# Kernel tuning notes

Hardware: AMD Instinct MI355X
Metric: run time of the kernel (lower is better)

## Reference

```python
import jax, jax.numpy as jnp
import numpy as np

D_MODEL, N_HEAD, N_KV_HEAD, D_HEAD = 1024, 16, 4, 64


def rotate_half(x):
    x1, x2 = x[..., : x.shape[-1] // 2], x[..., x.shape[-1] // 2:]
    return jnp.concatenate((-x2, x1), axis=-1)


def rope_cos_sin(seq_len, dim, dtype=jnp.float32):
    inv_freq = 1.0 / (10000.0 ** (jnp.arange(0, dim, 2, dtype=jnp.float32) / dim))
    t = jnp.arange(seq_len, dtype=jnp.float32)
    freqs = jnp.einsum('i,j->ij', t, inv_freq)          # [S, dim/2]
    emb = jnp.concatenate((freqs, freqs), axis=-1)       # [S, dim]
    return jnp.cos(emb).astype(dtype), jnp.sin(emb).astype(dtype)


def setup_inputs() -> dict:
    key = jax.random.key(0)
    ks = jax.random.split(key, 5)
    B, S = 2, 2048
    scale = 0.02
    return {
        'x': jax.random.normal(ks[0], (B, S, D_MODEL), dtype=jnp.float32),
        'Wq': jax.random.normal(ks[1], (D_MODEL, N_HEAD * D_HEAD), dtype=jnp.float32) * scale,
        'Wk': jax.random.normal(ks[2], (D_MODEL, N_KV_HEAD * D_HEAD), dtype=jnp.float32) * scale,
        'Wv': jax.random.normal(ks[3], (D_MODEL, N_KV_HEAD * D_HEAD), dtype=jnp.float32) * scale,
        'Wo': jax.random.normal(ks[4], (N_HEAD * D_HEAD, D_MODEL), dtype=jnp.float32) * scale,
    }


def reference(x, Wq, Wk, Wv, Wo):
    B, S, _ = x.shape
    scale = 1.0 / np.sqrt(D_HEAD)
    # projections -> [B, H, S, Dh]
    q = (x @ Wq).reshape(B, S, N_HEAD, D_HEAD).transpose(0, 2, 1, 3)
    k = (x @ Wk).reshape(B, S, N_KV_HEAD, D_HEAD).transpose(0, 2, 1, 3)
    v = (x @ Wv).reshape(B, S, N_KV_HEAD, D_HEAD).transpose(0, 2, 1, 3)
    cos, sin = rope_cos_sin(S, D_HEAD, x.dtype)          # [S, Dh]
    q = q * cos + rotate_half(q) * sin
    k = k * cos + rotate_half(k) * sin
    rep = N_HEAD // N_KV_HEAD
    k = jnp.repeat(k, rep, axis=1)                       # [B, H, S, Dh]
    v = jnp.repeat(v, rep, axis=1)
    scores = jnp.einsum('bhqd,bhkd->bhqk', q, k) * scale # [B, H, S, S]
    causal = jnp.triu(jnp.ones((S, S), dtype=bool), k=1)
    scores = jnp.where(causal, -jnp.inf, scores)
    probs = jax.nn.softmax(scores, axis=-1)
    ctx = jnp.einsum('bhqk,bhkd->bhqd', probs, v)        # [B, H, S, Dh]
    ctx = ctx.transpose(0, 2, 1, 3).reshape(B, S, N_HEAD * D_HEAD)
    return ctx @ Wo
```

## Files before the change

### kernel.cpp

```cpp
#include <hip/hip_runtime.h>
#include <hip/hip_bf16.h>
#include <cstdint>
#include <math.h>

#define S_LEN 2048
#define DM 1024
#define NQKV 1536
#define MROWS 4096
#define BKT 64

typedef __attribute__((ext_vector_type(8))) short short8;
typedef __attribute__((ext_vector_type(4))) float f32x4;
typedef __attribute__((ext_vector_type(16))) float f32x16;

#define QFOLD 0.18033688011112042f

__device__ __forceinline__ short f2bf(float x) {
  union { float f; uint32_t u; } v; v.f = x;
  uint32_t r = (v.u + 0x7fffu + ((v.u >> 16) & 1u)) >> 16;
  return (short)(uint16_t)r;
}

__device__ __forceinline__ uint32_t pk2(float a, float b) {
  __hip_bfloat162 h = __float22bfloat162_rn(make_float2(a, b));
  union { __hip_bfloat162 h2; uint32_t u; } cv; cv.h2 = h;
  return cv.u;
}

__global__ __launch_bounds__(256) void prep(const float* __restrict__ x,
    const float* __restrict__ Wq, const float* __restrict__ Wk,
    const float* __restrict__ Wv, const float* __restrict__ Wo,
    short* __restrict__ Xb, short* __restrict__ WcatT, short* __restrict__ WoT,
    float2* __restrict__ tab) {
  __shared__ short T[64 * 72];
  const int bb = blockIdx.x;
  const int tid = threadIdx.x;
  if (bb < 4096) {
    const int i = bb * 256 + tid;
    float4 v = ((const float4*)x)[i];
    short4 o;
    o.x = f2bf(v.x); o.y = f2bf(v.y); o.z = f2bf(v.z); o.w = f2bf(v.w);
    ((short4*)Xb)[i] = o;
    return;
  }
  if (bb >= 4736) {
    const int gid = (bb - 4736) * 256 + tid;
    #pragma unroll
    for (int e = 0; e < 4; ++e) {
      const int ii = gid + e * 16384;
      const int s = ii >> 5, j = ii & 31;
      const float inv = exp2f(-(float)j * 0.41524101186092029f);
      const float ang = (float)s * inv;
      tab[ii] = make_float2(cosf(ang), sinf(ang));
    }
    return;
  }
  const float* src; short* dst; int R, C, t2 = bb - 4096;
  if (t2 < 256)      { src = Wq; dst = WcatT;                        R = 1024; C = 1024; }
  else if (t2 < 320) { t2 -= 256; src = Wk; dst = WcatT + (size_t)1024*1024; R = 1024; C = 256; }
  else if (t2 < 384) { t2 -= 320; src = Wv; dst = WcatT + (size_t)1280*1024; R = 1024; C = 256; }
  else               { t2 -= 384; src = Wo; dst = WoT;               R = 1024; C = 1024; }
  const int r0 = (t2 & 15) * 64, c0 = (t2 >> 4) * 64;
  #pragma unroll
  for (int i = 0; i < 4; ++i) {
    int chunk = tid + i * 256;
    int r = chunk >> 4, cc = (chunk & 15) * 4;
    float4 v = *(const float4*)&src[(size_t)(r0 + r) * C + c0 + cc];
    T[(cc + 0) * 72 + r] = f2bf(v.x);
    T[(cc + 1) * 72 + r] = f2bf(v.y);
    T[(cc + 2) * 72 + r] = f2bf(v.z);
    T[(cc + 3) * 72 + r] = f2bf(v.w);
  }
  __syncthreads();
  #pragma unroll
  for (int i = 0; i < 2; ++i) {
    int chunk = tid + i * 256;
    int rr = chunk >> 3, kk = (chunk & 7) * 8;
    *(uint4*)&dst[(size_t)(c0 + rr) * R + r0 + kk] = *(uint4*)&T[rr * 72 + kk];
  }
}

template<int BMT, int BNT>
__global__ __launch_bounds__(256) void gemm_bf16_t(const short* __restrict__ A,
    const short* __restrict__ BT, float* __restrict__ C, int M, int N, int K) {
  constexpr int MI = BMT / 32, NI = BNT / 32;
  __shared__ short As[BMT * BKT];
  __shared__ short Bs[BNT * BKT];
  const int tid = threadIdx.x;
  const int wave = tid >> 6, lane = tid & 63;
  const int quad = lane >> 4, l15 = lane & 15;
  const int wm = (wave >> 1) * (BMT / 2), wn = (wave & 1) * (BNT / 2);
  const int m0 = blockIdx.y * BMT, n0 = blockIdx.x * BNT;
  const int rA = wave * (BMT / 4) + (lane >> 3);
  const int rB = wave * (BNT / 4) + (lane >> 3);
  const int scol = (lane & 7) * 8;

  f32x4 acc[MI][NI] = {};

  for (int k0 = 0; k0 < K; k0 += BKT) {
    __syncthreads();
    #pragma unroll
    for (int j = 0; j < MI; ++j)
      __builtin_amdgcn_global_load_lds(
          (const __attribute__((address_space(1))) void*)&A[(size_t)(m0 + rA + j * 8) * K + k0 + scol],
          (__attribute__((address_space(3))) void*)&As[(wave * MI + j) * 512],
          16, 0, 0);
    #pragma unroll
    for (int j = 0; j < NI; ++j)
      __builtin_amdgcn_global_load_lds(
          (const __attribute__((address_space(1))) void*)&BT[(size_t)(n0 + rB + j * 8) * K + k0 + scol],
          (__attribute__((address_space(3))) void*)&Bs[(wave * NI + j) * 512],
          16, 0, 0);
    __syncthreads();
    #pragma unroll
    for (int ks = 0; ks < 2; ++ks) {
      short8 af[MI], bfr[NI];
      #pragma unroll
      for (int mi = 0; mi < MI; ++mi)
        af[mi] = *(const short8*)&As[(wm + mi*16 + l15)*BKT + ks*32 + quad*8];
      #pragma unroll
      for (int ni = 0; ni < NI; ++ni)
        bfr[ni] = *(const short8*)&Bs[(wn + ni*16 + l15)*BKT + ks*32 + quad*8];
      #pragma unroll
      for (int mi = 0; mi < MI; ++mi)
        #pragma unroll
        for (int ni = 0; ni < NI; ++ni)
          acc[mi][ni] = __builtin_amdgcn_mfma_f32_16x16x32_bf16(af[mi], bfr[ni], acc[mi][ni], 0, 0, 0);
    }
  }
  #pragma unroll
  for (int mi = 0; mi < MI; ++mi)
    #pragma unroll
    for (int ni = 0; ni < NI; ++ni)
      #pragma unroll
      for (int r = 0; r < 4; ++r)
        C[(size_t)(m0 + wm + mi*16 + quad*4 + r)*N + (n0 + wn + ni*16 + l15)] = acc[mi][ni][r];
}

__global__ __launch_bounds__(256, 3) void gemm_qkv(const short* __restrict__ A,
    const short* __restrict__ BT, const float2* __restrict__ tab,
    short* __restrict__ Qb, short* __restrict__ Kb, short* __restrict__ Vt) {
  constexpr int MI = 2, NI = 4;
  __shared__ short SM[12288];
  short* As = SM;
  short* Bs = SM + 4096;
  const int tid = threadIdx.x;
  const int wave = tid >> 6, lane = tid & 63;
  const int quad = lane >> 4, l15 = lane & 15;
  const int wm = (wave >> 1) * 32, wn = (wave & 1) * 64;
  const int m0 = blockIdx.y * 64, n0 = blockIdx.x * 128;
  const int rA = wave * 16 + (lane >> 3);
  const int rB = wave * 32 + (lane >> 3);
  const int scol = (lane & 7) * 8;

  f32x4 acc[MI][NI] = {};

  for (int k0 = 0; k0 < DM; k0 += BKT) {
    __syncthreads();
    #pragma unroll
    for (int j = 0; j < MI; ++j)
      __builtin_amdgcn_global_load_lds(
          (const __attribute__((address_space(1))) void*)&A[(size_t)(m0 + rA + j * 8) * DM + k0 + scol],
          (__attribute__((address_space(3))) void*)&As[(wave * MI + j) * 512],
          16, 0, 0);
    #pragma unroll
    for (int j = 0; j < NI; ++j)
      __builtin_amdgcn_global_load_lds(
          (const __attribute__((address_space(1))) void*)&BT[(size_t)(n0 + rB + j * 8) * DM + k0 + scol],
          (__attribute__((address_space(3))) void*)&Bs[(wave * NI + j) * 512],
          16, 0, 0);
    __syncthreads();
    #pragma unroll
    for (int ks = 0; ks < 2; ++ks) {
      short8 af[MI], bfr[NI];
      #pragma unroll
      for (int mi = 0; mi < MI; ++mi)
        af[mi] = *(const short8*)&As[(wm + mi*16 + l15)*BKT + ks*32 + quad*8];
      #pragma unroll
      for (int ni = 0; ni < NI; ++ni)
        bfr[ni] = *(const short8*)&Bs[(wn + ni*16 + l15)*BKT + ks*32 + quad*8];
      #pragma unroll
      for (int mi = 0; mi < MI; ++mi)
        #pragma unroll
        for (int ni = 0; ni < NI; ++ni)
          acc[mi][ni] = __builtin_amdgcn_mfma_f32_16x16x32_bf16(af[mi], bfr[ni], acc[mi][ni], 0, 0, 0);
    }
  }

  const int c0 = n0 + wn;
  if (n0 < 1024) {
    #pragma unroll
    for (int mi = 0; mi < MI; ++mi)
      #pragma unroll
      for (int r = 0; r < 4; ++r) {
        const int row = m0 + wm + mi*16 + quad*4 + r;
        const int s = row & (S_LEN - 1);
        #pragma unroll
        for (int ni = 0; ni < 2; ++ni) {
          const int j = ni*16 + l15;
          const float2 cn = tab[s*32 + j];
          const float x1 = acc[mi][ni][r], x2 = acc[mi][ni+2][r];
          Qb[(size_t)row*1024 + c0 + j]      = f2bf((x1*cn.x - x2*cn.y) * QFOLD);
          Qb[(size_t)row*1024 + c0 + j + 32] = f2bf((x2*cn.x + x1*cn.y) * QFOLD);
        }
      }
  } else if (n0 < 1280) {
    const int hh = (c0 - 1024) >> 6;
    #pragma unroll
    for (int mi = 0; mi < MI; ++mi)
      #pragma unroll
      for (int r = 0; r < 4; ++r) {
        const int row = m0 + wm + mi*16 + quad*4 + r;
        const int s = row & (S_LEN - 1);
        const int sw = (s & 7) << 3;
        #pragma unroll
        for (int ni = 0; ni < 2; ++ni) {
          const int j = ni*16 + l15;
          const float2 cn = tab[s*32 + j];
          const float x1 = acc[mi][ni][r], x2 = acc[mi][ni+2][r];
          Kb[(size_t)row*256 + hh*64 + (j ^ sw)]        = f2bf(x1*cn.x - x2*cn.y);
          Kb[(size_t)row*256 + hh*64 + ((j + 32) ^ sw)] = f2bf(x2*cn.x + x1*cn.y);
        }
      }
  } else {
    __syncthreads();
    #pragma unroll
    for (int mi = 0; mi < MI; ++mi)
      #pragma unroll
      for (int ni = 0; ni < NI; ++ni) {
        short4 p;
        p.x = f2bf(acc[mi][ni][0]); p.y = f2bf(acc[mi][ni][1]);
        p.z = f2bf(acc[mi][ni][2]); p.w = f2bf(acc[mi][ni][3]);
        *(short4*)&SM[(wn + ni*16 + l15)*80 + wm + mi*16 + quad*4] = p;
      }
    __syncthreads();
    const int b_ = m0 >> 11, sbase = m0 & (S_LEN - 1);
    #pragma unroll
    for (int i = 0; i < 4; ++i) {
      const int chunk = tid + i * 256;
      const int vl = chunk >> 3;
      const int kk = (chunk & 7) * 8;
      const int vcol = (n0 - 1280) + vl;
      const int kvh = vcol >> 6, dd = vcol & 63;
      uint4 v = *(uint4*)&SM[vl*80 + kk];
      *(uint4*)&Vt[((size_t)((b_*4 + kvh)*64 + dd))*S_LEN + sbase + (kk ^ ((dd & 7) << 3))] = v;
    }
  }
}

__global__ __launch_bounds__(256, 3) void fattn12(const short* __restrict__ Qb,
    const short* __restrict__ Kb, const short* __restrict__ Vt, short* __restrict__ Ctx) {
  __shared__ short SMEM[24576];
  const int idx = blockIdx.x;
  const int h   = idx & 15;
  const int b   = (idx >> 4) & 1;
  const int jt  = 31 - (idx >> 5);
  const int kvh = h >> 2;
  const int tid = threadIdx.x, wav = tid >> 6, lane = tid & 63;
  const int l31 = lane & 31, hi = lane >> 5;
  const int qs = wav & 1, g = wav >> 1;
  const int sx = (l31 & 7) << 3;
  const size_t qbase  = (size_t)b * S_LEN * 1024;
  const size_t kbase  = (size_t)b * S_LEN * 256;
  const size_t vtbase = (size_t)(b * 4 + kvh) * 64 * S_LEN;

  const short* kptr = Kb + kbase + (size_t)(wav * 16 + (lane >> 3)) * 256 + kvh * 64 + (lane & 7) * 8;
  const short* vptr = Vt + vtbase + (size_t)(wav * 16 + (lane >> 3)) * 2048 + (lane & 7) * 8;

#define STAGE(u) do { \
    const int bi_ = (u) % 3; \
    const short* kp_ = kptr + (size_t)(u) * 16384; \
    const short* vp_ = vptr + (u) * 64; \
    short* kd_ = &SMEM[bi_ * 8192 + wav * 1024]; \
    short* vd_ = &SMEM[bi_ * 8192 + 4096 + wav * 1024]; \
    _Pragma("unroll") \
    for (int i_ = 0; i_ < 2; ++i_) { \
      __builtin_amdgcn_global_load_lds((const __attribute__((address_space(1))) void*)(kp_ + i_ * 2048), \
          (__attribute__((address_space(3))) void*)(kd_ + i_ * 512), 16, 0, 0); \
      __builtin_amdgcn_global_load_lds((const __attribute__((address_space(1))) void*)(vp_ + i_ * 16384), \
          (__attribute__((address_space(3))) void*)(vd_ + i_ * 512), 16, 0, 0); \
    } \
  } while (0)

  const int q0 = jt * 64;
  const int ntiles = jt + 1;
  const int qg = q0 + qs * 32 + l31;

  short8 qf[4];
  {
    const short* qp = &Qb[qbase + (size_t)qg * 1024 + h * 64 + hi * 8];
    #pragma unroll
    for (int ks = 0; ks < 4; ++ks) qf[ks] = *(const short8*)(qp + ks * 16);
  }

  f32x16 O0 = {}, O1 = {};
  f32x16 P0 = {}, P1 = {};
  float la0 = 0.f, la1 = 0.f, la2 = 0.f, la3 = 0.f;

  STAGE(0);
  if (ntiles > 1) STAGE(1);

  for (int t = 0; t < ntiles; ++t) {
    const int k0 = t * 64;
    const int rem = ntiles - 1 - t;
    if (rem >= 1) { asm volatile("s_waitcnt vmcnt(4)" ::: "memory"); }
    else          { asm volatile("s_waitcnt vmcnt(0)" ::: "memory"); }
    __builtin_amdgcn_sched_barrier(0);
    __builtin_amdgcn_s_barrier();
    if (t + 2 < ntiles) STAGE(t + 2);

    const short* ks_ = &SMEM[(t % 3) * 8192];
    const short* vs_ = &SMEM[(t % 3) * 8192 + 4096];

    f32x16 sc;
    __builtin_amdgcn_s_setprio(1);
    {
      const int r = g * 32 + l31;
      short8 kf0 = *(const short8*)&ks_[r * 64 + ((0 * 16 + hi * 8) ^ sx)];
      short8 kf1 = *(const short8*)&ks_[r * 64 + ((1 * 16 + hi * 8) ^ sx)];
      short8 kf2 = *(const short8*)&ks_[r * 64 + ((2 * 16 + hi * 8) ^ sx)];
      short8 kf3 = *(const short8*)&ks_[r * 64 + ((3 * 16 + hi * 8) ^ sx)];
      f32x16 a0 = {}, a1 = {};
      a0 = __builtin_amdgcn_mfma_f32_32x32x16_bf16(kf0, qf[0], a0, 0, 0, 0);
      a1 = __builtin_amdgcn_mfma_f32_32x32x16_bf16(kf2, qf[2], a1, 0, 0, 0);
      a0 = __builtin_amdgcn_mfma_f32_32x32x16_bf16(kf1, qf[1], a0, 0, 0, 0);
      a1 = __builtin_amdgcn_mfma_f32_32x32x16_bf16(kf3, qf[3], a1, 0, 0, 0);
      #pragma unroll
      for (int r2 = 0; r2 < 16; ++r2) sc[r2] = a0[r2] + a1[r2];
    }
    __builtin_amdgcn_s_setprio(0);

    if (t == ntiles - 1) {
      #pragma unroll
      for (int r = 0; r < 16; ++r) {
        const int kvg = k0 + g * 32 + (r & 3) + 8 * (r >> 2) + 4 * hi;
        if (kvg > qg) sc[r] = -1e30f;
      }
    }

    short8 af[2];
    {
      #pragma unroll
      for (int r = 0; r < 16; ++r) sc[r] = exp2f(sc[r]);
      la0 += (sc[0] + sc[1]) + (sc[2] + sc[3]);
      la1 += (sc[4] + sc[5]) + (sc[6] + sc[7]);
      la2 += (sc[8] + sc[9]) + (sc[10] + sc[11]);
      la3 += (sc[12] + sc[13]) + (sc[14] + sc[15]);
      #pragma unroll
      for (int st = 0; st < 2; ++st) {
        uint32_t x0 = pk2(sc[st * 8 + 0], sc[st * 8 + 1]);
        uint32_t x1 = pk2(sc[st * 8 + 2], sc[st * 8 + 3]);
        uint32_t x2 = pk2(sc[st * 8 + 4], sc[st * 8 + 5]);
        uint32_t x3 = pk2(sc[st * 8 + 6], sc[st * 8 + 7]);
        asm("v_permlane32_swap_b32 %0, %1" : "+v"(x0), "+v"(x2));
        asm("v_permlane32_swap_b32 %0, %1" : "+v"(x1), "+v"(x3));
        union { short8 s8; uint32_t u[4]; } cv;
        cv.u[0] = x0; cv.u[1] = x1; cv.u[2] = x2; cv.u[3] = x3;
        af[st] = cv.s8;
      }
    }

    __builtin_amdgcn_s_setprio(1);
    {
      const int co0 = g * 32 + hi * 8;
      const int co1 = g * 32 + 16 + hi * 8;
      short8 bv00 = *(const short8*)&vs_[l31 * 64 + (co0 ^ sx)];
      short8 bv01 = *(const short8*)&vs_[(32 + l31) * 64 + (co0 ^ sx)];
      short8 bv10 = *(const short8*)&vs_[l31 * 64 + (co1 ^ sx)];
      short8 bv11 = *(const short8*)&vs_[(32 + l31) * 64 + (co1 ^ sx)];
      O0 = __builtin_amdgcn_mfma_f32_32x32x16_bf16(af[0], bv00, O0, 0, 0, 0);
      O1 = __builtin_amdgcn_mfma_f32_32x32x16_bf16(af[0], bv01, O1, 0, 0, 0);
      P0 = __builtin_amdgcn_mfma_f32_32x32x16_bf16(af[1], bv10, P0, 0, 0, 0);
      P1 = __builtin_amdgcn_mfma_f32_32x32x16_bf16(af[1], bv11, P1, 0, 0, 0);
    }
    __builtin_amdgcn_s_setprio(0);
  }

  #pragma unroll
  for (int r = 0; r < 16; ++r) { O0[r] += P0[r]; O1[r] += P1[r]; }

  float ll = (la0 + la1) + (la2 + la3);
  ll += __shfl_xor(ll, 32, 64);
  __syncthreads();

  float* Os = (float*)SMEM;
  float* Ls = (float*)SMEM + 2 * 64 * 33;
  if (g == 1) {
    float* op = &Os[(qs * 64 + lane) * 33];
    #pragma unroll
    for (int r = 0; r < 16; ++r) { op[r] = O0[r]; op[16 + r] = O1[r]; }
    Ls[qs * 64 + lane] = ll;
  }
  __syncthreads();
  if (g == 0) {
    const float* op = &Os[(qs * 64 + lane) * 33];
    ll += Ls[qs * 64 + lane];
    #pragma unroll
    for (int r = 0; r < 16; ++r) { O0[r] += op[r]; O1[r] += op[16 + r]; }
    const float inv = 1.0f / ll;
    #pragma unroll
    for (int r = 0; r < 16; ++r) {
      const int crow = (r & 3) + 8 * (r >> 2) + 4 * hi;
      const float invr = __shfl(inv, crow, 64);
      const size_t o = qbase + (size_t)(q0 + qs * 32 + crow) * 1024 + h * 64;
      Ctx[o + l31]      = f2bf(O0[r] * invr);
      Ctx[o + 32 + l31] = f2bf(O1[r] * invr);
    }
  }
#undef STAGE
}

extern "C" void kernel_launch(void* const* d_in, const int* in_sizes, int n_in,
                              void* d_out, int out_size, void* d_ws, size_t ws_size,
                              hipStream_t stream) {
  const float* x  = (const float*)d_in[0];
  const float* Wq = (const float*)d_in[1];
  const float* Wk = (const float*)d_in[2];
  const float* Wv = (const float*)d_in[3];
  const float* Wo = (const float*)d_in[4];
  float* out = (float*)d_out;

  char* w = (char*)d_ws;
  short*  Xb    = (short*)w;   w += (size_t)MROWS * DM * 2;
  short*  WcatT = (short*)w;   w += (size_t)NQKV * DM * 2;
  short*  WoT   = (short*)w;   w += (size_t)DM * DM * 2;
  short*  Qbuf  = (short*)w;   w += (size_t)MROWS * DM * 2;
  short*  Kbuf  = (short*)w;   w += (size_t)MROWS * 256 * 2;
  short*  Vt    = (short*)w;   w += (size_t)8 * 64 * S_LEN * 2;
  short*  Ctx   = (short*)w;   w += (size_t)MROWS * DM * 2;
  float2* tab   = (float2*)w;  w += (size_t)S_LEN * 32 * 8;

  prep<<<dim3(4800), dim3(256), 0, stream>>>(x, Wq, Wk, Wv, Wo, Xb, WcatT, WoT, tab);

  gemm_qkv<<<dim3(NQKV / 128, MROWS / 64), dim3(256), 0, stream>>>(Xb, WcatT, tab, Qbuf, Kbuf, Vt);
  fattn12<<<dim3(1024), dim3(256), 0, stream>>>(Qbuf, Kbuf, Vt, Ctx);
  gemm_bf16_t<64,128><<<dim3(DM / 128, MROWS / 64), dim3(256), 0, stream>>>(Ctx, WoT, out, MROWS, DM, DM);
}
```

Measured before the change: 164.2 us.

## Share KV tiles across the four GQA query heads in one attention block

```diff
diff --git a/kernel.cpp b/kernel.cpp
--- a/kernel.cpp
+++ b/kernel.cpp
@@ -248,43 +248,43 @@
   }
 }
 
-__global__ __launch_bounds__(256, 3) void fattn12(const short* __restrict__ Qb,
+__global__ __launch_bounds__(256, 3) void fattn13(const short* __restrict__ Qb,
     const short* __restrict__ Kb, const short* __restrict__ Vt, short* __restrict__ Ctx) {
   __shared__ short SMEM[24576];
   const int idx = blockIdx.x;
-  const int h   = idx & 15;
-  const int b   = (idx >> 4) & 1;
-  const int jt  = 31 - (idx >> 5);
-  const int kvh = h >> 2;
+  const int kk_ = (idx & 255) >> 3;
+  const int jt  = (idx >> 8) ? kk_ : 63 - kk_;
+  const int b   = (idx >> 2) & 1;
+  const int kvh = idx & 3;
   const int tid = threadIdx.x, wav = tid >> 6, lane = tid & 63;
   const int l31 = lane & 31, hi = lane >> 5;
-  const int qs = wav & 1, g = wav >> 1;
+  const int h = kvh * 4 + wav;
   const int sx = (l31 & 7) << 3;
   const size_t qbase  = (size_t)b * S_LEN * 1024;
   const size_t kbase  = (size_t)b * S_LEN * 256;
   const size_t vtbase = (size_t)(b * 4 + kvh) * 64 * S_LEN;
 
-  const short* kptr = Kb + kbase + (size_t)(wav * 16 + (lane >> 3)) * 256 + kvh * 64 + (lane & 7) * 8;
-  const short* vptr = Vt + vtbase + (size_t)(wav * 16 + (lane >> 3)) * 2048 + (lane & 7) * 8;
+  const short* kptr = Kb + kbase + (size_t)(tid >> 3) * 256 + kvh * 64 + (tid & 7) * 8;
+  const short* vptr = Vt + vtbase + (size_t)(tid >> 3) * 2048 + (tid & 7) * 8;
 
 #define STAGE(u) do { \
     const int bi_ = (u) % 3; \
     const short* kp_ = kptr + (size_t)(u) * 16384; \
     const short* vp_ = vptr + (u) * 64; \
-    short* kd_ = &SMEM[bi_ * 8192 + wav * 1024]; \
-    short* vd_ = &SMEM[bi_ * 8192 + 4096 + wav * 1024]; \
+    short* kd_ = &SMEM[bi_ * 8192 + tid * 8]; \
+    short* vd_ = &SMEM[bi_ * 8192 + 4096 + tid * 8]; \
     _Pragma("unroll") \
     for (int i_ = 0; i_ < 2; ++i_) { \
-      __builtin_amdgcn_global_load_lds((const __attribute__((address_space(1))) void*)(kp_ + i_ * 2048), \
-          (__attribute__((address_space(3))) void*)(kd_ + i_ * 512), 16, 0, 0); \
-      __builtin_amdgcn_global_load_lds((const __attribute__((address_space(1))) void*)(vp_ + i_ * 16384), \
-          (__attribute__((address_space(3))) void*)(vd_ + i_ * 512), 16, 0, 0); \
+      __builtin_amdgcn_global_load_lds((const __attribute__((address_space(1))) void*)(kp_ + i_ * 8192), \
+          (__attribute__((address_space(3))) void*)(kd_ + i_ * 2048), 16, 0, 0); \
+      __builtin_amdgcn_global_load_lds((const __attribute__((address_space(1))) void*)(vp_ + i_ * 65536), \
+          (__attribute__((address_space(3))) void*)(vd_ + i_ * 2048), 16, 0, 0); \
     } \
   } while (0)
 
-  const int q0 = jt * 64;
-  const int ntiles = jt + 1;
-  const int qg = q0 + qs * 32 + l31;
+  const int q0 = jt * 32;
+  const int ntiles = (jt >> 1) + 1;
+  const int qg = q0 + l31;
 
   short8 qf[4];
   {
@@ -294,7 +294,6 @@
   }
 
   f32x16 O0 = {}, O1 = {};
-  f32x16 P0 = {}, P1 = {};
   float la0 = 0.f, la1 = 0.f, la2 = 0.f, la3 = 0.f;
 
   STAGE(0);
@@ -312,100 +311,76 @@
     const short* ks_ = &SMEM[(t % 3) * 8192];
     const short* vs_ = &SMEM[(t % 3) * 8192 + 4096];
 
-    f32x16 sc;
+    f32x16 sc[2];
     __builtin_amdgcn_s_setprio(1);
-    {
-      const int r = g * 32 + l31;
-      short8 kf0 = *(const short8*)&ks_[r * 64 + ((0 * 16 + hi * 8) ^ sx)];
-      short8 kf1 = *(const short8*)&ks_[r * 64 + ((1 * 16 + hi * 8) ^ sx)];
-      short8 kf2 = *(const short8*)&ks_[r * 64 + ((2 * 16 + hi * 8) ^ sx)];
-      short8 kf3 = *(const short8*)&ks_[r * 64 + ((3 * 16 + hi * 8) ^ sx)];
-      f32x16 a0 = {}, a1 = {};
-      a0 = __builtin_amdgcn_mfma_f32_32x32x16_bf16(kf0, qf[0], a0, 0, 0, 0);
-      a1 = __builtin_amdgcn_mfma_f32_32x32x16_bf16(kf2, qf[2], a1, 0, 0, 0);
-      a0 = __builtin_amdgcn_mfma_f32_32x32x16_bf16(kf1, qf[1], a0, 0, 0, 0);
-      a1 = __builtin_amdgcn_mfma_f32_32x32x16_bf16(kf3, qf[3], a1, 0, 0, 0);
-      #pragma unroll
-      for (int r2 = 0; r2 < 16; ++r2) sc[r2] = a0[r2] + a1[r2];
+    #pragma unroll
+    for (int kt = 0; kt < 2; ++kt) {
+      const int r = kt * 32 + l31;
+      f32x16 a = {};
+      #pragma unroll
+      for (int ks2 = 0; ks2 < 4; ++ks2) {
+        short8 kf = *(const short8*)&ks_[r * 64 + ((ks2 * 16 + hi * 8) ^ sx)];
+        a = __builtin_amdgcn_mfma_f32_32x32x16_bf16(kf, qf[ks2], a, 0, 0, 0);
+      }
+      sc[kt] = a;
     }
     __builtin_amdgcn_s_setprio(0);
 
     if (t == ntiles - 1) {
       #pragma unroll
-      for (int r = 0; r < 16; ++r) {
-        const int kvg = k0 + g * 32 + (r & 3) + 8 * (r >> 2) + 4 * hi;
-        if (kvg > qg) sc[r] = -1e30f;
-      }
-    }
-
-    short8 af[2];
-    {
-      #pragma unroll
-      for (int r = 0; r < 16; ++r) sc[r] = exp2f(sc[r]);
-      la0 += (sc[0] + sc[1]) + (sc[2] + sc[3]);
-      la1 += (sc[4] + sc[5]) + (sc[6] + sc[7]);
-      la2 += (sc[8] + sc[9]) + (sc[10] + sc[11]);
-      la3 += (sc[12] + sc[13]) + (sc[14] + sc[15]);
+      for (int kt = 0; kt < 2; ++kt)
+        #pragma unroll
+        for (int r = 0; r < 16; ++r) {
+          const int kvg = k0 + kt * 32 + (r & 3) + 8 * (r >> 2) + 4 * hi;
+          if (kvg > qg) sc[kt][r] = -1e30f;
+        }
+    }
+
+    short8 af[4];
+    #pragma unroll
+    for (int kt = 0; kt < 2; ++kt) {
+      #pragma unroll
+      for (int r = 0; r < 16; ++r) sc[kt][r] = exp2f(sc[kt][r]);
+      la0 += (sc[kt][0] + sc[kt][1]) + (sc[kt][2] + sc[kt][3]);
+      la1 += (sc[kt][4] + sc[kt][5]) + (sc[kt][6] + sc[kt][7]);
+      la2 += (sc[kt][8] + sc[kt][9]) + (sc[kt][10] + sc[kt][11]);
+      la3 += (sc[kt][12] + sc[kt][13]) + (sc[kt][14] + sc[kt][15]);
       #pragma unroll
       for (int st = 0; st < 2; ++st) {
-        uint32_t x0 = pk2(sc[st * 8 + 0], sc[st * 8 + 1]);
-        uint32_t x1 = pk2(sc[st * 8 + 2], sc[st * 8 + 3]);
-        uint32_t x2 = pk2(sc[st * 8 + 4], sc[st * 8 + 5]);
-        uint32_t x3 = pk2(sc[st * 8 + 6], sc[st * 8 + 7]);
+        uint32_t x0 = pk2(sc[kt][st * 8 + 0], sc[kt][st * 8 + 1]);
+        uint32_t x1 = pk2(sc[kt][st * 8 + 2], sc[kt][st * 8 + 3]);
+        uint32_t x2 = pk2(sc[kt][st * 8 + 4], sc[kt][st * 8 + 5]);
+        uint32_t x3 = pk2(sc[kt][st * 8 + 6], sc[kt][st * 8 + 7]);
         asm("v_permlane32_swap_b32 %0, %1" : "+v"(x0), "+v"(x2));
         asm("v_permlane32_swap_b32 %0, %1" : "+v"(x1), "+v"(x3));
         union { short8 s8; uint32_t u[4]; } cv;
         cv.u[0] = x0; cv.u[1] = x1; cv.u[2] = x2; cv.u[3] = x3;
-        af[st] = cv.s8;
+        af[kt * 2 + st] = cv.s8;
       }
     }
 
     __builtin_amdgcn_s_setprio(1);
-    {
-      const int co0 = g * 32 + hi * 8;
-      const int co1 = g * 32 + 16 + hi * 8;
-      short8 bv00 = *(const short8*)&vs_[l31 * 64 + (co0 ^ sx)];
-      short8 bv01 = *(const short8*)&vs_[(32 + l31) * 64 + (co0 ^ sx)];
-      short8 bv10 = *(const short8*)&vs_[l31 * 64 + (co1 ^ sx)];
-      short8 bv11 = *(const short8*)&vs_[(32 + l31) * 64 + (co1 ^ sx)];
-      O0 = __builtin_amdgcn_mfma_f32_32x32x16_bf16(af[0], bv00, O0, 0, 0, 0);
-      O1 = __builtin_amdgcn_mfma_f32_32x32x16_bf16(af[0], bv01, O1, 0, 0, 0);
-      P0 = __builtin_amdgcn_mfma_f32_32x32x16_bf16(af[1], bv10, P0, 0, 0, 0);
-      P1 = __builtin_amdgcn_mfma_f32_32x32x16_bf16(af[1], bv11, P1, 0, 0, 0);
+    #pragma unroll
+    for (int s = 0; s < 4; ++s) {
+      const int co = s * 16 + hi * 8;
+      short8 bv0 = *(const short8*)&vs_[l31 * 64 + (co ^ sx)];
+      O0 = __builtin_amdgcn_mfma_f32_32x32x16_bf16(af[s], bv0, O0, 0, 0, 0);
+      short8 bv1 = *(const short8*)&vs_[(32 + l31) * 64 + (co ^ sx)];
+      O1 = __builtin_amdgcn_mfma_f32_32x32x16_bf16(af[s], bv1, O1, 0, 0, 0);
     }
     __builtin_amdgcn_s_setprio(0);
   }
-
-  #pragma unroll
-  for (int r = 0; r < 16; ++r) { O0[r] += P0[r]; O1[r] += P1[r]; }
 
   float ll = (la0 + la1) + (la2 + la3);
   ll += __shfl_xor(ll, 32, 64);
-  __syncthreads();
-
-  float* Os = (float*)SMEM;
-  float* Ls = (float*)SMEM + 2 * 64 * 33;
-  if (g == 1) {
-    float* op = &Os[(qs * 64 + lane) * 33];
-    #pragma unroll
-    for (int r = 0; r < 16; ++r) { op[r] = O0[r]; op[16 + r] = O1[r]; }
-    Ls[qs * 64 + lane] = ll;
-  }
-  __syncthreads();
-  if (g == 0) {
-    const float* op = &Os[(qs * 64 + lane) * 33];
-    ll += Ls[qs * 64 + lane];
-    #pragma unroll
-    for (int r = 0; r < 16; ++r) { O0[r] += op[r]; O1[r] += op[16 + r]; }
-    const float inv = 1.0f / ll;
-    #pragma unroll
-    for (int r = 0; r < 16; ++r) {
-      const int crow = (r & 3) + 8 * (r >> 2) + 4 * hi;
-      const float invr = __shfl(inv, crow, 64);
-      const size_t o = qbase + (size_t)(q0 + qs * 32 + crow) * 1024 + h * 64;
-      Ctx[o + l31]      = f2bf(O0[r] * invr);
-      Ctx[o + 32 + l31] = f2bf(O1[r] * invr);
-    }
+  const float inv = 1.0f / ll;
+  #pragma unroll
+  for (int r = 0; r < 16; ++r) {
+    const int crow = (r & 3) + 8 * (r >> 2) + 4 * hi;
+    const float invr = __shfl(inv, crow, 64);
+    const size_t o = qbase + (size_t)(q0 + crow) * 1024 + h * 64;
+    Ctx[o + l31]      = f2bf(O0[r] * invr);
+    Ctx[o + 32 + l31] = f2bf(O1[r] * invr);
   }
 #undef STAGE
 }
@@ -433,6 +408,6 @@
   prep<<<dim3(4800), dim3(256), 0, stream>>>(x, Wq, Wk, Wv, Wo, Xb, WcatT, WoT, tab);
 
   gemm_qkv<<<dim3(NQKV / 128, MROWS / 64), dim3(256), 0, stream>>>(Xb, WcatT, tab, Qbuf, Kbuf, Vt);
-  fattn12<<<dim3(1024), dim3(256), 0, stream>>>(Qbuf, Kbuf, Vt, Ctx);
+  fattn13<<<dim3(512), dim3(256), 0, stream>>>(Qbuf, Kbuf, Vt, Ctx);
   gemm_bf16_t<64,128><<<dim3(DM / 128, MROWS / 64), dim3(256), 0, stream>>>(Ctx, WoT, out, MROWS, DM, DM);
 }
```

Result: slower. 167.5 us (+2.0%).
